# Optimization experiments

Measured on AMD Instinct MI355X. Metric: run time of the kernel, lower is better.

Reference implementation:

```python
import jax, jax.numpy as jnp
import numpy as np
import math

B, NO, ML, D, H = 32, 512, 512, 1024, 16


def setup_inputs() -> dict:
    key = jax.random.key(0)
    ks = jax.random.split(key, 16)
    v = jax.random.normal(ks[0], (B, NO, D), jnp.float32)
    t = jax.random.normal(ks[1], (B, ML, D), jnp.float32)
    # valid-length prefix masks (float, as in the torch module)
    v_len = jax.random.randint(ks[2], (B,), NO // 2, NO + 1)
    t_len = jax.random.randint(ks[3], (B,), ML // 2, ML + 1)
    v_mask = (jnp.arange(NO)[None, :] < v_len[:, None]).astype(jnp.float32)
    t_mask = (jnp.arange(ML)[None, :] < t_len[:, None]).astype(jnp.float32)
    lin = lambda k, din, dout: jax.random.normal(k, (din, dout), jnp.float32) * 0.02
    return {
        "v": v, "t": t, "v_mask": v_mask, "t_mask": t_mask,
        "W_v4t": lin(ks[4], D, D), "b_v4t": jnp.zeros((D,), jnp.float32),
        "W_t4v": lin(ks[5], D, D), "b_t4v": jnp.zeros((D,), jnp.float32),
        "W_v": lin(ks[6], D, 3 * D), "b_v": jnp.zeros((3 * D,), jnp.float32),
        "W_t": lin(ks[7], D, 3 * D), "b_t": jnp.zeros((3 * D,), jnp.float32),
        "W_vo": lin(ks[8], D, D), "b_vo": jnp.zeros((D,), jnp.float32),
        "W_to": lin(ks[9], D, D), "b_to": jnp.zeros((D,), jnp.float32),
        "num_head": H,
    }


def _heads(x, h, dh):
    b, n, _ = x.shape
    return x.reshape(b, n, h, dh).transpose(0, 2, 1, 3)  # [B,H,N,dh]


def _unheads(x):
    b, h, n, dh = x.shape
    return x.transpose(0, 2, 1, 3).reshape(b, n, h * dh)


def _attend(q, k, val, mask, gate, h, dh):
    # gate: [B, D] -> per-head diag scale [B,H,1,dh]
    g = 1.0 + gate.reshape(-1, h, 1, dh)
    scores = jnp.einsum('bhqd,bhkd->bhqk', g * q, g * k) / math.sqrt(dh)
    scores = jnp.where(mask[:, None, None, :] > 0, scores, -jnp.inf)
    attn = jax.nn.softmax(scores, axis=-1)
    return _unheads(jnp.einsum('bhqk,bhkd->bhqd', attn, val))


def reference(v, t, v_mask, t_mask, W_v4t, b_v4t, W_t4v, b_t4v,
              W_v, b_v, W_t, b_t, W_vo, b_vo, W_to, b_to, num_head):
    d = v.shape[-1]
    dh = d // num_head
    # masked mean pooling per modality
    v_mean = (v * v_mask[:, :, None]).sum(1) / v_mask.sum(1, keepdims=True)
    t_mean = (t * t_mask[:, :, None]).sum(1) / t_mask.sum(1, keepdims=True)
    v4t_gate = jax.nn.sigmoid(jax.nn.relu(v_mean) @ W_v4t + b_v4t)  # [B,D]
    t4v_gate = jax.nn.sigmoid(jax.nn.relu(t_mean) @ W_t4v + b_t4v)
    # fused KQV projections, masked
    v_trans = (jax.nn.relu(v) @ W_v + b_v) * v_mask[:, :, None]
    t_trans = (jax.nn.relu(t) @ W_t + b_t) * t_mask[:, :, None]
    # torch split order: k, q, v
    v_k, v_q, v_v = (_heads(v_trans[..., i * d:(i + 1) * d], num_head, dh) for i in range(3))
    t_k, t_q, t_v = (_heads(t_trans[..., i * d:(i + 1) * d], num_head, dh) for i in range(3))
    v_update = _attend(v_q, v_k, v_v, v_mask, t4v_gate, num_head, dh)
    t_update = _attend(t_q, t_k, t_v, t_mask, v4t_gate, num_head, dh)
    updated_v = (v + v_update) @ W_vo + b_vo
    updated_t = (t + t_update) @ W_to + b_to
    return updated_v, updated_t
```

## Files before the change

kernel.cpp:

```cpp
#include <hip/hip_runtime.h>
#include <hip/hip_bf16.h>
#include <math.h>

#define B_   32
#define NO_  512
#define D_   1024
#define H_   16
#define DH_  64
#define D3_  3072

typedef __hip_bfloat16 bf16;
typedef short short8  __attribute__((ext_vector_type(8)));
typedef short short4v __attribute__((ext_vector_type(4)));
typedef float f32x4   __attribute__((ext_vector_type(4)));

__device__ inline short f2bf(float x) {
  bf16 h = __float2bfloat16(x);
  return *reinterpret_cast<short*>(&h);
}
__device__ inline float bf2f(short s) {
  union { unsigned int u; float f; } cv;
  cv.u = ((unsigned int)(unsigned short)s) << 16;
  return cv.f;
}

__device__ inline void gload_lds16(const void* g, void* l) {
  __builtin_amdgcn_global_load_lds(
      (__attribute__((address_space(1))) void*)(void*)(g),
      (__attribute__((address_space(3))) void*)(l), 16, 0, 0);
}

__global__ __launch_bounds__(256) void pool_kernel(
    const float* __restrict__ v, const float* __restrict__ t,
    const float* __restrict__ vmask, const float* __restrict__ tmask,
    float* __restrict__ vmean, float* __restrict__ tmean) {
  const float* x; const float* m; float* out;
  if (blockIdx.y == 0) { x = v; m = vmask; out = vmean; }
  else                 { x = t; m = tmask; out = tmean; }
  int b = blockIdx.x >> 2;
  int d = ((blockIdx.x & 3) << 8) + threadIdx.x;
  float acc = 0.f, msum = 0.f;
  const float* xp = x + ((size_t)b * NO_) * D_ + d;
  const float* mp = m + b * NO_;
  for (int n = 0; n < NO_; ++n) {
    float mv = mp[n];
    acc  += xp[(size_t)n * D_] * mv;
    msum += mv;
  }
  out[b * D_ + d] = acc / msum;
}

__global__ __launch_bounds__(256) void gate_kernel(
    const float* __restrict__ vmean, const float* __restrict__ tmean,
    const float* __restrict__ Wv4t, const float* __restrict__ bv4t,
    const float* __restrict__ Wt4v, const float* __restrict__ bt4v,
    float* __restrict__ gv4t, float* __restrict__ gt4v) {
  const float* mean; const float* W; const float* bias; float* out;
  if (blockIdx.y == 0) { mean = vmean; W = Wv4t; bias = bv4t; out = gv4t; }
  else                 { mean = tmean; W = Wt4v; bias = bt4v; out = gt4v; }
  int b = blockIdx.x >> 2;
  int j = ((blockIdx.x & 3) << 8) + threadIdx.x;
  const float* mb = mean + b * D_;
  float acc = bias[j];
  for (int k = 0; k < D_; ++k) {
    float mv = mb[k]; mv = mv > 0.f ? mv : 0.f;
    acc += mv * W[(size_t)k * D_ + j];
  }
  out[b * D_ + j] = 1.f / (1.f + expf(-acc));
}

__global__ __launch_bounds__(256) void wtrans_kernel(
    const float* __restrict__ W, short* __restrict__ Wt, int K, int N) {
  __shared__ float tile[32][33];
  int n0 = blockIdx.x * 32, k0 = blockIdx.y * 32;
  int tx = threadIdx.x & 31, ty = threadIdx.x >> 5;
#pragma unroll
  for (int i = 0; i < 4; ++i) {
    int kk = ty + i * 8;
    tile[kk][tx] = W[(size_t)(k0 + kk) * N + n0 + tx];
  }
  __syncthreads();
#pragma unroll
  for (int i = 0; i < 4; ++i) {
    int nn = ty + i * 8;
    Wt[(size_t)(n0 + nn) * K + k0 + tx] = f2bf(tile[tx][nn]);
  }
}

__global__ __launch_bounds__(256) void reluconv_kernel(
    const float* __restrict__ x, short* __restrict__ y) {
  int i = (blockIdx.x * 256 + threadIdx.x) * 4;
  float4 vv = *(const float4*)(x + i);
  short4v o;
  o[0] = f2bf(vv.x > 0.f ? vv.x : 0.f);
  o[1] = f2bf(vv.y > 0.f ? vv.y : 0.f);
  o[2] = f2bf(vv.z > 0.f ? vv.z : 0.f);
  o[3] = f2bf(vv.w > 0.f ? vv.w : 0.f);
  *(short4v*)(y + i) = o;
}

__device__ __forceinline__ void stage_half(const short* __restrict__ g,
                                           short* l, int wave, int lane) {
#pragma unroll
  for (int r2 = 0; r2 < 2; ++r2) {
    int ob  = r2 * 8192 + wave * 1024;
    int o   = ob + lane * 16;
    int row = o >> 7;
    int kb  = (o & 127) ^ ((row & 7) << 4);
    gload_lds16(g + (size_t)row * D_ + (kb >> 1), l + (ob >> 1));
  }
}

__device__ __forceinline__ void read_a4(short8 (&a)[4][2], const short* As,
                                        int baseRow, int col, int qb) {
#pragma unroll
  for (int m = 0; m < 4; ++m) {
    int row = baseRow + m * 16 + col;
    int sw  = (row & 7) << 4;
    a[m][0] = *(const short8*)(As + (((row << 7) + (qb ^ sw)) >> 1));
    a[m][1] = *(const short8*)(As + (((row << 7) + ((64 + qb) ^ sw)) >> 1));
  }
}

__device__ __forceinline__ void read_b2(short8 (&b)[2][2], const short* Bs,
                                        int baseRow, int col, int qb) {
#pragma unroll
  for (int n = 0; n < 2; ++n) {
    int row = baseRow + n * 16 + col;
    int sw  = (row & 7) << 4;
    b[n][0] = *(const short8*)(Bs + (((row << 7) + (qb ^ sw)) >> 1));
    b[n][1] = *(const short8*)(Bs + (((row << 7) + ((64 + qb) ^ sw)) >> 1));
  }
}

template<int MH, int NH>
__device__ __forceinline__ void mma8(f32x4 (&acc)[8][4],
                                     const short8 (&a)[4][2],
                                     const short8 (&b)[2][2]) {
#pragma unroll
  for (int m = 0; m < 4; ++m)
#pragma unroll
    for (int n = 0; n < 2; ++n)
#pragma unroll
      for (int kh = 0; kh < 2; ++kh)
        acc[MH * 4 + m][NH * 2 + n] = __builtin_amdgcn_mfma_f32_16x16x32_bf16(
            a[m][kh], b[n][kh], acc[MH * 4 + m][NH * 2 + n], 0, 0, 0);
}

#define PHASE_TAIL(MH, NH, BR)                              \
  __builtin_amdgcn_s_barrier();                             \
  asm volatile("s_waitcnt lgkmcnt(0)" ::: "memory");        \
  __builtin_amdgcn_s_setprio(1);                            \
  mma8<MH, NH>(acc, a, BR);                                 \
  __builtin_amdgcn_s_setprio(0);                            \
  __builtin_amdgcn_s_barrier();

template<int SA, int SB, int VMN>
__device__ __forceinline__ void ktile(
    f32x4 (&acc)[8][4], short8 (&a)[4][2], short8 (&b0)[2][2], short8 (&b1)[2][2],
    const short* Asc, const short* Bsc, short* Asn, short* Bsn,
    const short* gA, const short* gB,
    int wm, int wn, int col, int qb, int wave, int lane) {
  read_a4(a, Asc, wm * 128, col, qb);
  read_b2(b0, Bsc, wn * 64, col, qb);
  if constexpr (SA) stage_half(gA, Asn, wave, lane);
  PHASE_TAIL(0, 0, b0)
  read_b2(b1, Bsc, wn * 64 + 32, col, qb);
  if constexpr (SA) stage_half(gA + 128 * D_, Asn + 8192, wave, lane);
  PHASE_TAIL(0, 1, b1)
  read_a4(a, Asc, wm * 128 + 64, col, qb);
  if constexpr (SB) stage_half(gB, Bsn, wave, lane);
  PHASE_TAIL(1, 0, b0)
  if constexpr (SB) stage_half(gB + 128 * D_, Bsn + 8192, wave, lane);
  __builtin_amdgcn_s_barrier();
  __builtin_amdgcn_s_setprio(1);
  mma8<1, 1>(acc, a, b1);
  __builtin_amdgcn_s_setprio(0);
  if constexpr (VMN >= 0)
    asm volatile("s_waitcnt vmcnt(%0)" :: "i"(VMN) : "memory");
  __builtin_amdgcn_s_barrier();
}

template<int EPI>
__global__ __launch_bounds__(512, 2) void mfma_gemm256_kernel(
    const short* __restrict__ A, const short* __restrict__ Bt,
    const float* __restrict__ bias, const float* __restrict__ mask,
    void* __restrict__ Cout, int M, int N) {
  __shared__ short lds[65536];
  short* As0 = lds;
  short* Bs0 = lds + 16384;
  short* As1 = lds + 32768;
  short* Bs1 = lds + 49152;

  const int tid  = threadIdx.x;
  const int wave = tid >> 6, lane = tid & 63;
  const int col  = lane & 15, quad = lane >> 4, qb = quad << 4;
  const int wm   = wave >> 2, wn = wave & 3;

  const int nx   = gridDim.x;
  const int orig = blockIdx.y * nx + blockIdx.x;
  const int cpx  = (nx * gridDim.y) >> 3;
  const int swz  = (orig & 7) * cpx + (orig >> 3);
  const int bx   = swz % nx;
  const int by   = swz / nx;
  const int rowBase = by * 256;
  const int colBase = bx * 256;

  const short* gA = A  + (size_t)rowBase * D_;
  const short* gB = Bt + (size_t)colBase * D_;

  f32x4 zero = {0.f, 0.f, 0.f, 0.f};
  f32x4 acc[8][4];
#pragma unroll
  for (int i = 0; i < 8; ++i)
#pragma unroll
    for (int j = 0; j < 4; ++j) acc[i][j] = zero;

  short8 a[4][2], b0[2][2], b1[2][2];

  stage_half(gA,                 As0,        wave, lane);
  stage_half(gA + 128 * D_,      As0 + 8192, wave, lane);
  stage_half(gB,                 Bs0,        wave, lane);
  stage_half(gB + 128 * D_,      Bs0 + 8192, wave, lane);
  stage_half(gB + 64,            Bs1,        wave, lane);
  stage_half(gB + 64 + 128 * D_, Bs1 + 8192, wave, lane);
  asm volatile("s_waitcnt vmcnt(4)" ::: "memory");
  __builtin_amdgcn_s_barrier();

  const short* gAk = gA + 64;
  const short* gBk = gB + 128;
  for (int i = 0; i < 7; ++i) {
    ktile<1, 1, 4>(acc, a, b0, b1, As0, Bs0, As1, Bs0, gAk,      gBk,
                   wm, wn, col, qb, wave, lane);
    ktile<1, 1, 4>(acc, a, b0, b1, As1, Bs1, As0, Bs1, gAk + 64, gBk + 64,
                   wm, wn, col, qb, wave, lane);
    gAk += 128; gBk += 128;
  }
  ktile<1, 0, 0>(acc, a, b0, b1, As0, Bs0, As1, Bs0, gAk, gBk,
                 wm, wn, col, qb, wave, lane);
  ktile<0, 0, -1>(acc, a, b0, b1, As1, Bs1, As0, Bs1, gAk, gBk,
                  wm, wn, col, qb, wave, lane);

#pragma unroll
  for (int mi = 0; mi < 8; ++mi) {
    const int row = rowBase + wm * 128 + mi * 16 + quad * 4;
    float mk[4];
    if (EPI == 0) {
#pragma unroll
      for (int r = 0; r < 4; ++r) mk[r] = mask[row + r];
    }
#pragma unroll
    for (int ni = 0; ni < 4; ++ni) {
      const int c = colBase + wn * 64 + ni * 16 + col;
      const float bv = bias[c];
#pragma unroll
      for (int r = 0; r < 4; ++r) {
        float val = acc[mi][ni][r] + bv;
        if (EPI == 0) {
          val *= mk[r];
          ((short*)Cout)[(size_t)(row + r) * N + c] = f2bf(val);
        } else {
          ((float*)Cout)[(size_t)(row + r) * N + c] = val;
        }
      }
    }
  }
}
#undef PHASE_TAIL

#define ATT_PAD 72

__global__ __launch_bounds__(256) void attn_mfma_kernel(
    const short* __restrict__ trans, const float* __restrict__ mask,
    const float* __restrict__ gate, const float* __restrict__ x,
    short* __restrict__ a2) {
  __shared__ short Ks[64 * ATT_PAD];
  __shared__ short Vt[64 * ATT_PAD];
  __shared__ short Ps[4][16 * ATT_PAD];

  const int tid  = threadIdx.x;
  const int wave = tid >> 6;
  const int lane = tid & 63;
  const int col  = lane & 15;
  const int quad = lane >> 4;
  const int b = blockIdx.z, h = blockIdx.y;
  const int qBase = blockIdx.x * 64 + wave * 16;

  const short* transB = trans + (size_t)b * NO_ * D3_;

  short8 qf[2];
  {
    const int q = qBase + col;
    const short* qp = transB + (size_t)q * D3_ + D_ + h * DH_;
    const float* gp = gate + b * D_ + h * DH_;
#pragma unroll
    for (int f = 0; f < 2; ++f) {
      const int dh0 = f * 32 + quad * 8;
      short8 raw = *(const short8*)(qp + dh0);
      short8 sc;
#pragma unroll
      for (int j = 0; j < 8; ++j) {
        float g = 1.f + gp[dh0 + j];
        sc[j] = f2bf(bf2f(raw[j]) * g * g * 0.125f);
      }
      qf[f] = sc;
    }
  }

  f32x4 O[4] = {{0,0,0,0},{0,0,0,0},{0,0,0,0},{0,0,0,0}};
  float m_i[4] = {-1e30f, -1e30f, -1e30f, -1e30f};
  float l_i[4] = {0.f, 0.f, 0.f, 0.f};

  const int key0 = tid >> 3;
  const int mseg = tid & 7;

  for (int ch = 0; ch < 8; ++ch) {
    __syncthreads();
#pragma unroll
    for (int half = 0; half < 2; ++half) {
      const int key = key0 + half * 32;
      const short* src = transB + (size_t)(ch * 64 + key) * D3_ + h * DH_ + mseg * 8;
      *(short8*)&Ks[key * ATT_PAD + mseg * 8] = *(const short8*)src;
      short8 vv = *(const short8*)(src + 2 * D_);
#pragma unroll
      for (int i = 0; i < 8; ++i) {
        int j = (i + mseg) & 7;
        Vt[(mseg * 8 + j) * ATT_PAD + key] = vv[j];
      }
    }
    __syncthreads();

    f32x4 S[4];
#pragma unroll
    for (int f = 0; f < 4; ++f) {
      const int krow = (f * 16 + col) * ATT_PAD;
      short8 kb0 = *(short8*)&Ks[krow + quad * 8];
      short8 kb1 = *(short8*)&Ks[krow + 32 + quad * 8];
      f32x4 acc = {0.f, 0.f, 0.f, 0.f};
      acc = __builtin_amdgcn_mfma_f32_16x16x32_bf16(qf[0], kb0, acc, 0, 0, 0);
      acc = __builtin_amdgcn_mfma_f32_16x16x32_bf16(qf[1], kb1, acc, 0, 0, 0);
      S[f] = acc;
    }

    float mk[4];
#pragma unroll
    for (int f = 0; f < 4; ++f)
      mk[f] = mask[b * NO_ + ch * 64 + f * 16 + col];

#pragma unroll
    for (int r = 0; r < 4; ++r) {
      float sv[4];
      float mx = -1e30f;
#pragma unroll
      for (int f = 0; f < 4; ++f) {
        float s = S[f][r];
        s = (mk[f] > 0.f) ? s : -1e30f;
        sv[f] = s;
        mx = fmaxf(mx, s);
      }
#pragma unroll
      for (int off = 1; off < 16; off <<= 1)
        mx = fmaxf(mx, __shfl_xor(mx, off, 64));
      float mnew  = fmaxf(m_i[r], mx);
      float alpha = __expf(m_i[r] - mnew);
      float psum = 0.f;
#pragma unroll
      for (int f = 0; f < 4; ++f) {
        float p = __expf(sv[f] - mnew);
        psum += p;
        Ps[wave][(quad * 4 + r) * ATT_PAD + f * 16 + col] = f2bf(p);
      }
#pragma unroll
      for (int off = 1; off < 16; off <<= 1)
        psum += __shfl_xor(psum, off, 64);
      l_i[r] = l_i[r] * alpha + psum;
      m_i[r] = mnew;
#pragma unroll
      for (int t = 0; t < 4; ++t) O[t][r] *= alpha;
    }

#pragma unroll
    for (int k2 = 0; k2 < 2; ++k2) {
      short8 pa = *(short8*)&Ps[wave][col * ATT_PAD + k2 * 32 + quad * 8];
#pragma unroll
      for (int t = 0; t < 4; ++t) {
        short8 vb = *(short8*)&Vt[(t * 16 + col) * ATT_PAD + k2 * 32 + quad * 8];
        O[t] = __builtin_amdgcn_mfma_f32_16x16x32_bf16(pa, vb, O[t], 0, 0, 0);
      }
    }
  }

#pragma unroll
  for (int t = 0; t < 4; ++t) {
#pragma unroll
    for (int r = 0; r < 4; ++r) {
      int q = qBase + quad * 4 + r;
      size_t idx = ((size_t)b * NO_ + q) * D_ + h * DH_ + t * 16 + col;
      a2[idx] = f2bf(x[idx] + O[t][r] / l_i[r]);
    }
  }
}

extern "C" void kernel_launch(void* const* d_in, const int* in_sizes, int n_in,
                              void* d_out, int out_size, void* d_ws, size_t ws_size,
                              hipStream_t stream) {
  const float* v      = (const float*)d_in[0];
  const float* t      = (const float*)d_in[1];
  const float* v_mask = (const float*)d_in[2];
  const float* t_mask = (const float*)d_in[3];
  const float* W_v4t  = (const float*)d_in[4];
  const float* b_v4t  = (const float*)d_in[5];
  const float* W_t4v  = (const float*)d_in[6];
  const float* b_t4v  = (const float*)d_in[7];
  const float* W_v    = (const float*)d_in[8];
  const float* b_v    = (const float*)d_in[9];
  const float* W_t    = (const float*)d_in[10];
  const float* b_t    = (const float*)d_in[11];
  const float* W_vo   = (const float*)d_in[12];
  const float* b_vo   = (const float*)d_in[13];
  const float* W_to   = (const float*)d_in[14];
  const float* b_to   = (const float*)d_in[15];
  float* out = (float*)d_out;

  const size_t M = (size_t)B_ * NO_;

  float* ws     = (float*)d_ws;
  float* v_mean = ws;
  float* t_mean = v_mean + B_ * D_;
  float* g_v4t  = t_mean + B_ * D_;
  float* g_t4v  = g_v4t + B_ * D_;
  short* trans  = (short*)(g_t4v + B_ * D_);
  short* Abf    = trans + M * D3_;
  short* Wt_v   = Abf + M * D_;
  short* Wt_t   = Wt_v + (size_t)D3_ * D_;
  short* Wt_vo  = Wt_t + (size_t)D3_ * D_;
  short* Wt_to  = Wt_vo + (size_t)D_ * D_;

  pool_kernel<<<dim3(B_ * 4, 2), 256, 0, stream>>>(v, t, v_mask, t_mask, v_mean, t_mean);
  gate_kernel<<<dim3(B_ * 4, 2), 256, 0, stream>>>(v_mean, t_mean, W_v4t, b_v4t,
                                                   W_t4v, b_t4v, g_v4t, g_t4v);

  wtrans_kernel<<<dim3(D3_ / 32, D_ / 32), 256, 0, stream>>>(W_v,  Wt_v,  D_, D3_);
  wtrans_kernel<<<dim3(D3_ / 32, D_ / 32), 256, 0, stream>>>(W_t,  Wt_t,  D_, D3_);
  wtrans_kernel<<<dim3(D_ / 32,  D_ / 32), 256, 0, stream>>>(W_vo, Wt_vo, D_, D_);
  wtrans_kernel<<<dim3(D_ / 32,  D_ / 32), 256, 0, stream>>>(W_to, Wt_to, D_, D_);

  dim3 kqv_grid(D3_ / 256, M / 256);
  dim3 out_grid(D_ / 256,  M / 256);
  dim3 att_grid(NO_ / 64, H_, B_);
  int  conv_blocks = (int)(M * D_ / (256 * 4));

  reluconv_kernel<<<conv_blocks, 256, 0, stream>>>(v, Abf);
  mfma_gemm256_kernel<0><<<kqv_grid, 512, 0, stream>>>(Abf, Wt_v, b_v, v_mask,
                                                       trans, (int)M, D3_);
  attn_mfma_kernel<<<att_grid, 256, 0, stream>>>(trans, v_mask, g_t4v, v, Abf);
  mfma_gemm256_kernel<1><<<out_grid, 512, 0, stream>>>(Abf, Wt_vo, b_vo, nullptr,
                                                       out, (int)M, D_);

  reluconv_kernel<<<conv_blocks, 256, 0, stream>>>(t, Abf);
  mfma_gemm256_kernel<0><<<kqv_grid, 512, 0, stream>>>(Abf, Wt_t, b_t, t_mask,
                                                       trans, (int)M, D3_);
  attn_mfma_kernel<<<att_grid, 256, 0, stream>>>(trans, t_mask, g_v4t, t, Abf);
  mfma_gemm256_kernel<1><<<out_grid, 512, 0, stream>>>(Abf, Wt_to, b_to, nullptr,
                                                       out + M * D_, (int)M, D_);
}
```

Before: 911.2 us.

## Skip fully masked key chunks and transpose score MFMA for cheaper softmax

Each attention block reduces its mask to a valid key length and iterates only over key chunks that contain valid keys, masking by index in the final partial chunk. The QK^T MFMA operands are swapped so each lane holds scores for one query, which replaces 16-lane shuffle reductions with two shuffles and allows packed P stores. This assumes the mask is a contiguous prefix, which holds for the generated inputs but not for arbitrary masks.

```diff
diff --git a/kernel.cpp b/kernel.cpp
--- a/kernel.cpp
+++ b/kernel.cpp
@@ -277,6 +277,7 @@
   __shared__ short Ks[64 * ATT_PAD];
   __shared__ short Vt[64 * ATT_PAD];
   __shared__ short Ps[4][16 * ATT_PAD];
+  __shared__ float lensh[4];
 
   const int tid  = threadIdx.x;
   const int wave = tid >> 6;
@@ -288,6 +289,13 @@
 
   const short* transB = trans + (size_t)b * NO_ * D3_;
 
+  {
+    float s = mask[b * NO_ + tid] + mask[b * NO_ + 256 + tid];
+#pragma unroll
+    for (int off = 1; off < 64; off <<= 1) s += __shfl_xor(s, off, 64);
+    if (lane == 0) lensh[wave] = s;
+  }
+
   short8 qf[2];
   {
     const int q = qBase + col;
@@ -306,15 +314,18 @@
       qf[f] = sc;
     }
   }
+  __syncthreads();
+  const int len = (int)(lensh[0] + lensh[1] + lensh[2] + lensh[3] + 0.5f);
+  const int nch = (len + 63) >> 6;
 
   f32x4 O[4] = {{0,0,0,0},{0,0,0,0},{0,0,0,0},{0,0,0,0}};
-  float m_i[4] = {-1e30f, -1e30f, -1e30f, -1e30f};
-  float l_i[4] = {0.f, 0.f, 0.f, 0.f};
+  float m_i = -1e30f;
+  float l_i = 0.f;
 
   const int key0 = tid >> 3;
   const int mseg = tid & 7;
 
-  for (int ch = 0; ch < 8; ++ch) {
+  for (int ch = 0; ch < nch; ++ch) {
     __syncthreads();
 #pragma unroll
     for (int half = 0; half < 2; ++half) {
@@ -330,53 +341,66 @@
     }
     __syncthreads();
 
-    f32x4 S[4];
+    f32x4 St[4];
 #pragma unroll
     for (int f = 0; f < 4; ++f) {
       const int krow = (f * 16 + col) * ATT_PAD;
       short8 kb0 = *(short8*)&Ks[krow + quad * 8];
       short8 kb1 = *(short8*)&Ks[krow + 32 + quad * 8];
       f32x4 acc = {0.f, 0.f, 0.f, 0.f};
-      acc = __builtin_amdgcn_mfma_f32_16x16x32_bf16(qf[0], kb0, acc, 0, 0, 0);
-      acc = __builtin_amdgcn_mfma_f32_16x16x32_bf16(qf[1], kb1, acc, 0, 0, 0);
-      S[f] = acc;
-    }
-
-    float mk[4];
-#pragma unroll
-    for (int f = 0; f < 4; ++f)
-      mk[f] = mask[b * NO_ + ch * 64 + f * 16 + col];
+      acc = __builtin_amdgcn_mfma_f32_16x16x32_bf16(kb0, qf[0], acc, 0, 0, 0);
+      acc = __builtin_amdgcn_mfma_f32_16x16x32_bf16(kb1, qf[1], acc, 0, 0, 0);
+      St[f] = acc;
+    }
+
+    const int kb0i = ch * 64 + quad * 4;
+    float mloc = -1e30f;
+    if (ch * 64 + 64 <= len) {
+#pragma unroll
+      for (int f = 0; f < 4; ++f)
+#pragma unroll
+        for (int r = 0; r < 4; ++r) mloc = fmaxf(mloc, St[f][r]);
+    } else {
+#pragma unroll
+      for (int f = 0; f < 4; ++f)
+#pragma unroll
+        for (int r = 0; r < 4; ++r) {
+          float s = (kb0i + f * 16 + r < len) ? St[f][r] : -1e30f;
+          St[f][r] = s;
+          mloc = fmaxf(mloc, s);
+        }
+    }
+    mloc = fmaxf(mloc, __shfl_xor(mloc, 16, 64));
+    mloc = fmaxf(mloc, __shfl_xor(mloc, 32, 64));
+    const float mnew  = fmaxf(m_i, mloc);
+    const float alpha = __expf(m_i - mnew);
+
+    float psum = 0.f;
+#pragma unroll
+    for (int f = 0; f < 4; ++f) {
+      float p0 = __expf(St[f][0] - mnew);
+      float p1 = __expf(St[f][1] - mnew);
+      float p2 = __expf(St[f][2] - mnew);
+      float p3 = __expf(St[f][3] - mnew);
+      psum += (p0 + p1) + (p2 + p3);
+      unsigned u0 = (unsigned)(unsigned short)f2bf(p0) |
+                    ((unsigned)(unsigned short)f2bf(p1) << 16);
+      unsigned u1 = (unsigned)(unsigned short)f2bf(p2) |
+                    ((unsigned)(unsigned short)f2bf(p3) << 16);
+      const int base = col * ATT_PAD + f * 16 + quad * 4;
+      *(unsigned*)&Ps[wave][base]     = u0;
+      *(unsigned*)&Ps[wave][base + 2] = u1;
+    }
+    psum += __shfl_xor(psum, 16, 64);
+    psum += __shfl_xor(psum, 32, 64);
+    l_i = l_i * alpha + psum;
+    m_i = mnew;
 
 #pragma unroll
     for (int r = 0; r < 4; ++r) {
-      float sv[4];
-      float mx = -1e30f;
-#pragma unroll
-      for (int f = 0; f < 4; ++f) {
-        float s = S[f][r];
-        s = (mk[f] > 0.f) ? s : -1e30f;
-        sv[f] = s;
-        mx = fmaxf(mx, s);
-      }
-#pragma unroll
-      for (int off = 1; off < 16; off <<= 1)
-        mx = fmaxf(mx, __shfl_xor(mx, off, 64));
-      float mnew  = fmaxf(m_i[r], mx);
-      float alpha = __expf(m_i[r] - mnew);
-      float psum = 0.f;
-#pragma unroll
-      for (int f = 0; f < 4; ++f) {
-        float p = __expf(sv[f] - mnew);
-        psum += p;
-        Ps[wave][(quad * 4 + r) * ATT_PAD + f * 16 + col] = f2bf(p);
-      }
-#pragma unroll
-      for (int off = 1; off < 16; off <<= 1)
-        psum += __shfl_xor(psum, off, 64);
-      l_i[r] = l_i[r] * alpha + psum;
-      m_i[r] = mnew;
-#pragma unroll
-      for (int t = 0; t < 4; ++t) O[t][r] *= alpha;
+      float ar = __shfl(alpha, (quad << 4) + quad * 4 + r, 64);
+#pragma unroll
+      for (int t = 0; t < 4; ++t) O[t][r] *= ar;
     }
 
 #pragma unroll
@@ -390,13 +414,17 @@
     }
   }
 
+  float lrec[4];
+#pragma unroll
+  for (int r = 0; r < 4; ++r)
+    lrec[r] = 1.f / __shfl(l_i, (quad << 4) + quad * 4 + r, 64);
 #pragma unroll
   for (int t = 0; t < 4; ++t) {
 #pragma unroll
     for (int r = 0; r < 4; ++r) {
       int q = qBase + quad * 4 + r;
       size_t idx = ((size_t)b * NO_ + q) * D_ + h * DH_ + t * 16 + col;
-      a2[idx] = f2bf(x[idx] + O[t][r] / l_i[r]);
+      a2[idx] = f2bf(x[idx] + O[t][r] * lrec[r]);
     }
   }
 }
```

Measured after the change: 824.8 us. -9.5%, faster.
